# Kernel tuning notes

Measured on AMD Instinct MI355X. Metric: run time of the kernel, lower is better.

## Reference

```python
import jax, jax.numpy as jnp
import numpy as np

LOG_2PI = float(np.log(2.0 * np.pi))


def setup_inputs() -> dict:
    key = jax.random.key(0)
    k1, k2, k3 = jax.random.split(key, 3)
    N, M, D = 8192, 4096, 784
    samples = jax.random.normal(k1, (N, D), dtype=jnp.float32)
    x = jax.random.normal(k2, (M, D), dtype=jnp.float32)
    # per-feature std, kept away from zero for numerical sanity
    std = jax.random.uniform(k3, (D,), dtype=jnp.float32, minval=0.5, maxval=1.5)
    return {"samples": samples, "x": x, "std": std}


def reference(samples, x, std):
    # Diagonal-Gaussian mixture log-prob:
    #   logp[n, m] = sum_d [ -0.5*((s_nd - x_md)/std_d)^2 - 0.5*log(2*pi) - log(std_d) ]
    # computed via the ||u||^2 + ||v||^2 - 2 u.v identity on std-scaled vectors
    # (mathematically identical to the torch broadcast, without the (N,M,D) tensor).
    N, D = samples.shape
    M = x.shape[0]
    u = samples / std  # (N, D)
    v = x / std        # (M, D)
    sq_dist = (
        jnp.sum(u * u, axis=1)[:, None]
        + jnp.sum(v * v, axis=1)[None, :]
        - 2.0 * jnp.einsum("nd,md->nm", u, v)
    )  # (N, M)
    log_const = -0.5 * D * LOG_2PI - jnp.sum(jnp.log(std))
    log_prob = -0.5 * sq_dist + log_const  # (N, M)
    # logsumexp over mixture components, minus log(M)
    return jax.nn.logsumexp(log_prob, axis=1) - jnp.log(jnp.asarray(M, dtype=samples.dtype))
```

## Files before the change

kernel.cpp:

```cpp
#include <hip/hip_runtime.h>
#include <cstdint>
#include <cstddef>


#define N_ROWS 8192
#define M_ROWS 4096
#define D_DIM  784
#define KPB    896
#define LOG2PI 1.8378770664093453f
#define LOGM   8.317766166719343f

typedef unsigned char u8;
typedef __attribute__((ext_vector_type(8))) int   i32x8;
typedef __attribute__((ext_vector_type(4))) float f32x4;

__device__ __forceinline__ void gld16(const u8* g, u8* l) {
    __builtin_amdgcn_global_load_lds(
        (__attribute__((address_space(1))) void*)(void*)g,
        (__attribute__((address_space(3))) void*)l, 16, 0, 0);
}

__global__ __launch_bounds__(256) void k_prep(const float* __restrict__ samples,
                                              const float* __restrict__ x,
                                              const float* __restrict__ stdv,
                                              u8* __restrict__ dst,
                                              float* __restrict__ norm) {
    const int wid = threadIdx.x >> 6, lane = threadIdx.x & 63;
    const int row0 = blockIdx.x * 8 + wid * 2;

    float4 rstd[4];
#pragma unroll
    for (int i = 0; i < 4; ++i) {
        int c = lane + 64 * i;
        rstd[i] = make_float4(1.f, 1.f, 1.f, 1.f);
        if (c < 196) {
            float4 d = ((const float4*)stdv)[c];
            rstd[i] = make_float4(1.f / d.x, 1.f / d.y, 1.f / d.z, 1.f / d.w);
        }
    }

#pragma unroll
    for (int rr = 0; rr < 2; ++rr) {
        const int row = row0 + rr;
        const float* src = (row < N_ROWS) ? samples + (size_t)row * D_DIM
                                          : x + (size_t)(row - N_ROWS) * D_DIM;
        unsigned* drow = (unsigned*)(dst + (size_t)row * KPB);
        float sq = 0.f;
#pragma unroll
        for (int i = 0; i < 4; ++i) {
            const int c = lane + 64 * i;
            if (c < 224) {
                unsigned p = 0;
                if (c < 196) {
                    float4 s = ((const float4*)src)[c];
                    float ux = s.x * rstd[i].x, uy = s.y * rstd[i].y;
                    float uz = s.z * rstd[i].z, uw = s.w * rstd[i].w;
                    p = __builtin_amdgcn_cvt_pk_fp8_f32(ux, uy, 0, false);
                    p = __builtin_amdgcn_cvt_pk_fp8_f32(uz, uw, p, true);
                    float r0 = __builtin_amdgcn_cvt_f32_fp8(p, 0);
                    float r1 = __builtin_amdgcn_cvt_f32_fp8(p, 1);
                    float r2 = __builtin_amdgcn_cvt_f32_fp8(p, 2);
                    float r3 = __builtin_amdgcn_cvt_f32_fp8(p, 3);
                    sq += r0 * r0 + r1 * r1 + r2 * r2 + r3 * r3;
                }
                drow[c] = p;
            }
        }
        for (int m = 32; m; m >>= 1) sq += __shfl_xor(sq, m);
        if (lane == 0) norm[row] = sq;
    }
}

__global__ __launch_bounds__(256) void k_gemm(const u8* __restrict__ U,
                                              const u8* __restrict__ V,
                                              const float* __restrict__ vnorm,
                                              float* __restrict__ pmax,
                                              float* __restrict__ psum) {
    __shared__ __align__(16) char smem[65536];
    float2* part = (float2*)smem;

    const int tid = threadIdx.x;
    const int lane = tid & 63;
    const int wid = tid >> 6;
    const int waveRow = wid >> 1;
    const int waveCol = wid & 1;
    const int bCol = blockIdx.x;
    const int bRow = blockIdx.y;
    const int g = lane >> 4, rl = lane & 15;

    const int r16 = lane >> 2, sl = lane & 3;
    const int gc16 = sl ^ ((r16 >> 1) & 3);
    const u8* ga[4]; const u8* gb[4]; int loff[4];
#pragma unroll
    for (int t = 0; t < 4; ++t) {
        const int lin = wid * 4 + t, h = lin & 1, rg = lin >> 1;
        ga[t] = U + (size_t)(bRow * 128 + rg * 16 + r16) * KPB + h * 64 + gc16 * 16;
        gb[t] = V + (size_t)(bCol * 128 + rg * 16 + r16) * KPB + h * 64 + gc16 * 16;
        loff[t] = h * 8192 + rg * 1024;
    }

    const int key = (rl >> 1) & 3;
    const int hA = (g >> 1) * 8192;
    const int slotLo = (2 * (g & 1)) ^ key;
    const int aoff = hA + (waveRow * 64 + rl) * 64 + slotLo * 16;
    const int boff = 16384 + hA + (waveCol * 64 + rl) * 64 + slotLo * 16;

    f32x4 acc[4][4];
#pragma unroll
    for (int i = 0; i < 4; ++i)
#pragma unroll
        for (int j = 0; j < 4; ++j) acc[i][j] = (f32x4){0.f, 0.f, 0.f, 0.f};

#pragma unroll
    for (int t = 0; t < 4; ++t) gld16(ga[t], (u8*)(smem + loff[t]));
#pragma unroll
    for (int t = 0; t < 4; ++t) gld16(gb[t], (u8*)(smem + 16384 + loff[t]));

#pragma unroll
    for (int kt = 0; kt < 7; ++kt) {
        if (kt < 6) {
            char* nb = smem + ((kt + 1) & 1) * 32768;
            const int k1 = (kt + 1) * 128;
#pragma unroll
            for (int t = 0; t < 4; ++t) gld16(ga[t] + k1, (u8*)(nb + loff[t]));
#pragma unroll
            for (int t = 0; t < 4; ++t) gld16(gb[t] + k1, (u8*)(nb + 16384 + loff[t]));
            __builtin_amdgcn_s_waitcnt(0x0F78);
        } else {
            __builtin_amdgcn_s_waitcnt(0x0F70);
        }
        __builtin_amdgcn_s_barrier();

        const char* base = smem + (kt & 1) * 32768;
        i32x8 a[4], b[4];
#pragma unroll
        for (int i = 0; i < 4; ++i) {
            int4 L = *(const int4*)(base + (aoff + i * 1024));
            int4 H = *(const int4*)(base + ((aoff + i * 1024) ^ 16));
            a[i] = (i32x8){L.x, L.y, L.z, L.w, H.x, H.y, H.z, H.w};
        }
#pragma unroll
        for (int j = 0; j < 4; ++j) {
            int4 L = *(const int4*)(base + (boff + j * 1024));
            int4 H = *(const int4*)(base + ((boff + j * 1024) ^ 16));
            b[j] = (i32x8){L.x, L.y, L.z, L.w, H.x, H.y, H.z, H.w};
        }
#pragma unroll
        for (int i = 0; i < 4; ++i)
#pragma unroll
            for (int j = 0; j < 4; ++j)
                acc[i][j] = __builtin_amdgcn_mfma_scale_f32_16x16x128_f8f6f4(
                    a[i], b[j], acc[i][j], 0 , 0 ,
                    0, 127 , 0, 127 );

        __builtin_amdgcn_s_barrier();
    }
    __syncthreads();

    float vn[4];
#pragma unroll
    for (int j = 0; j < 4; ++j) vn[j] = vnorm[bCol * 128 + waveCol * 64 + j * 16 + rl];

    const int prow0 = waveRow * 64 + g * 4;
    const int pcol = waveCol * 16 + rl;
#pragma unroll
    for (int i = 0; i < 4; ++i) {
#pragma unroll
        for (int rg = 0; rg < 4; ++rg) {
            float w0 = acc[i][0][rg] - 0.5f * vn[0];
            float w1 = acc[i][1][rg] - 0.5f * vn[1];
            float w2 = acc[i][2][rg] - 0.5f * vn[2];
            float w3 = acc[i][3][rg] - 0.5f * vn[3];
            float m = fmaxf(fmaxf(w0, w1), fmaxf(w2, w3));
            float s = __expf(w0 - m) + __expf(w1 - m) + __expf(w2 - m) + __expf(w3 - m);
            part[(prow0 + i * 16 + rg) * 33 + pcol] = make_float2(m, s);
        }
    }
    __syncthreads();
    if (tid < 128) {
        const float2* p = part + tid * 33;
        float m = p[0].x;
#pragma unroll
        for (int c = 1; c < 32; ++c) m = fmaxf(m, p[c].x);
        float s = 0.f;
#pragma unroll
        for (int c = 0; c < 32; ++c) { float2 q = p[c]; s += q.y * __expf(q.x - m); }
        size_t grow = (size_t)(bRow * 128 + tid);
        pmax[grow * 32 + bCol] = m;
        psum[grow * 32 + bCol] = s;
    }
}

__global__ __launch_bounds__(256) void k_final(const float* __restrict__ pmax,
                                               const float* __restrict__ psum,
                                               const float* __restrict__ norm,
                                               const float* __restrict__ stdv,
                                               float* __restrict__ out) {
    __shared__ float wsum[4];
    const int t = threadIdx.x;
    float ls = 0.f;
    for (int d = t; d < D_DIM; d += 256) ls += logf(stdv[d]);
    for (int m = 32; m; m >>= 1) ls += __shfl_xor(ls, m);
    if ((t & 63) == 0) wsum[t >> 6] = ls;
    __syncthreads();
    const float logc = -0.5f * (float)D_DIM * LOG2PI - (wsum[0] + wsum[1] + wsum[2] + wsum[3]);

    const int n = blockIdx.x * 256 + t;
    const float* pm = pmax + (size_t)n * 32;
    const float* ps = psum + (size_t)n * 32;
    float gm = pm[0];
#pragma unroll
    for (int c = 1; c < 32; ++c) gm = fmaxf(gm, pm[c]);
    float S = 0.f;
#pragma unroll
    for (int c = 0; c < 32; ++c) S += ps[c] * __expf(pm[c] - gm);
    out[n] = gm + logf(S) - 0.5f * norm[n] + logc - LOGM;
}

extern "C" void kernel_launch(void* const* d_in, const int* in_sizes, int n_in,
                              void* d_out, int out_size, void* d_ws, size_t ws_size,
                              hipStream_t stream) {
    const float* samples = (const float*)d_in[0];
    const float* x       = (const float*)d_in[1];
    const float* stdv    = (const float*)d_in[2];
    float* out = (float*)d_out;

    char* ws = (char*)d_ws;
    u8*    U    = (u8*)ws;
    u8*    V    = (u8*)(ws + 7340032);
    float* norm = (float*)(ws + 11010048);
    float* pmax = (float*)(ws + 11059200);
    float* psum = (float*)(ws + 12107776);

    k_prep<<<(N_ROWS + M_ROWS) / 8, 256, 0, stream>>>(samples, x, stdv, U, norm);
    k_gemm<<<dim3(M_ROWS / 128, N_ROWS / 128), 256, 0, stream>>>(U, V, norm + N_ROWS, pmax, psum);
    k_final<<<N_ROWS / 256, 256, 0, stream>>>(pmax, psum, norm, stdv, out);
}
```

Before: 126.0 us.

## Enlarge GEMM tile to 256x256 with 8 waves and deeper LDS pipeline

The fp8 MFMA GEMM goes from 128x128 tiles with 4 waves to 256x256 tiles with 8 waves, each wave computing 128x64. LDS grows to 128KB, split into four 64-wide K half-buffers, and K-step loads are issued further ahead. The MFMA loop is split into phases with barriers and s_setprio. The larger tile halves global traffic per FLOP and the number of partial logsumexp columns, at the cost of heavy LDS use, likely one block per CU, and only 512 blocks.

```diff
diff --git a/kernel.cpp b/kernel.cpp
--- a/kernel.cpp
+++ b/kernel.cpp
@@ -71,100 +71,107 @@
     }
 }
 
-__global__ __launch_bounds__(256) void k_gemm(const u8* __restrict__ U,
-                                              const u8* __restrict__ V,
-                                              const float* __restrict__ vnorm,
-                                              float* __restrict__ pmax,
-                                              float* __restrict__ psum) {
-    __shared__ __align__(16) char smem[65536];
+__global__ __launch_bounds__(512, 2) void k_gemm(const u8* __restrict__ U,
+                                                 const u8* __restrict__ V,
+                                                 const float* __restrict__ vnorm,
+                                                 float* __restrict__ pmax,
+                                                 float* __restrict__ psum) {
+    __shared__ __align__(16) char smem[131072];
     float2* part = (float2*)smem;
 
     const int tid = threadIdx.x;
     const int lane = tid & 63;
     const int wid = tid >> 6;
-    const int waveRow = wid >> 1;
-    const int waveCol = wid & 1;
+    const int waveRow = wid >> 2;
+    const int waveCol = wid & 3;
     const int bCol = blockIdx.x;
     const int bRow = blockIdx.y;
     const int g = lane >> 4, rl = lane & 15;
 
     const int r16 = lane >> 2, sl = lane & 3;
     const int gc16 = sl ^ ((r16 >> 1) & 3);
-    const u8* ga[4]; const u8* gb[4]; int loff[4];
-#pragma unroll
-    for (int t = 0; t < 4; ++t) {
-        const int lin = wid * 4 + t, h = lin & 1, rg = lin >> 1;
-        ga[t] = U + (size_t)(bRow * 128 + rg * 16 + r16) * KPB + h * 64 + gc16 * 16;
-        gb[t] = V + (size_t)(bCol * 128 + rg * 16 + r16) * KPB + h * 64 + gc16 * 16;
-        loff[t] = h * 8192 + rg * 1024;
+    const u8* gA[2]; const u8* gB[2]; int lo[2];
+#pragma unroll
+    for (int q = 0; q < 2; ++q) {
+        const int rg = wid * 2 + q;
+        gA[q] = U + (size_t)(bRow * 256 + rg * 16 + r16) * KPB + gc16 * 16;
+        gB[q] = V + (size_t)(bCol * 256 + rg * 16 + r16) * KPB + gc16 * 16;
+        lo[q] = rg * 1024;
     }
 
     const int key = (rl >> 1) & 3;
-    const int hA = (g >> 1) * 8192;
     const int slotLo = (2 * (g & 1)) ^ key;
-    const int aoff = hA + (waveRow * 64 + rl) * 64 + slotLo * 16;
-    const int boff = 16384 + hA + (waveCol * 64 + rl) * 64 + slotLo * 16;
-
-    f32x4 acc[4][4];
-#pragma unroll
-    for (int i = 0; i < 4; ++i)
+    const int aoff = (g >> 1) * 32768 + (waveRow * 128 + rl) * 64 + slotLo * 16;
+    const int boff = (g >> 1) * 32768 + 16384 + (waveCol * 64 + rl) * 64 + slotLo * 16;
+
+    f32x4 acc[8][4];
+#pragma unroll
+    for (int i = 0; i < 8; ++i)
 #pragma unroll
         for (int j = 0; j < 4; ++j) acc[i][j] = (f32x4){0.f, 0.f, 0.f, 0.f};
 
-#pragma unroll
-    for (int t = 0; t < 4; ++t) gld16(ga[t], (u8*)(smem + loff[t]));
-#pragma unroll
-    for (int t = 0; t < 4; ++t) gld16(gb[t], (u8*)(smem + 16384 + loff[t]));
-
-#pragma unroll
-    for (int kt = 0; kt < 7; ++kt) {
-        if (kt < 6) {
-            char* nb = smem + ((kt + 1) & 1) * 32768;
-            const int k1 = (kt + 1) * 128;
-#pragma unroll
-            for (int t = 0; t < 4; ++t) gld16(ga[t] + k1, (u8*)(nb + loff[t]));
-#pragma unroll
-            for (int t = 0; t < 4; ++t) gld16(gb[t] + k1, (u8*)(nb + 16384 + loff[t]));
-            __builtin_amdgcn_s_waitcnt(0x0F78);
-        } else {
-            __builtin_amdgcn_s_waitcnt(0x0F70);
-        }
+#define ISSUE(u) { \
+    u8* lb = (u8*)smem + ((u) & 3) * 32768; \
+    const int ko = (u) * 64; \
+    gld16(gA[0] + ko, lb + lo[0]); \
+    gld16(gB[0] + ko, lb + 16384 + lo[0]); \
+    gld16(gA[1] + ko, lb + lo[1]); \
+    gld16(gB[1] + ko, lb + 16384 + lo[1]); }
+
+    ISSUE(0); ISSUE(1); ISSUE(2);
+
+#pragma unroll
+    for (int T = 0; T < 7; ++T) {
+        if (T < 6) ISSUE(2 * T + 3);
+        if (T < 6) __builtin_amdgcn_s_waitcnt(0x0F78);
+        else       __builtin_amdgcn_s_waitcnt(0x0F70);
         __builtin_amdgcn_s_barrier();
 
-        const char* base = smem + (kt & 1) * 32768;
-        i32x8 a[4], b[4];
-#pragma unroll
-        for (int i = 0; i < 4; ++i) {
-            int4 L = *(const int4*)(base + (aoff + i * 1024));
-            int4 H = *(const int4*)(base + ((aoff + i * 1024) ^ 16));
-            a[i] = (i32x8){L.x, L.y, L.z, L.w, H.x, H.y, H.z, H.w};
-        }
-#pragma unroll
-        for (int j = 0; j < 4; ++j) {
-            int4 L = *(const int4*)(base + (boff + j * 1024));
-            int4 H = *(const int4*)(base + ((boff + j * 1024) ^ 16));
-            b[j] = (i32x8){L.x, L.y, L.z, L.w, H.x, H.y, H.z, H.w};
-        }
-#pragma unroll
-        for (int i = 0; i < 4; ++i)
-#pragma unroll
-            for (int j = 0; j < 4; ++j)
-                acc[i][j] = __builtin_amdgcn_mfma_scale_f32_16x16x128_f8f6f4(
-                    a[i], b[j], acc[i][j], 0 , 0 ,
-                    0, 127 , 0, 127 );
-
-        __builtin_amdgcn_s_barrier();
-    }
+        const char* base = smem + (T & 1) * 65536;
+        i32x8 b[4], a[2];
+#pragma unroll
+        for (int ph = 0; ph < 4; ++ph) {
+            if (ph == 0) {
+#pragma unroll
+                for (int j = 0; j < 4; ++j) {
+                    int4 L = *(const int4*)(base + (boff + j * 1024));
+                    int4 H = *(const int4*)(base + ((boff + j * 1024) ^ 16));
+                    b[j] = (i32x8){L.x, L.y, L.z, L.w, H.x, H.y, H.z, H.w};
+                }
+            }
+#pragma unroll
+            for (int t = 0; t < 2; ++t) {
+                const int i = ph * 2 + t;
+                int4 L = *(const int4*)(base + (aoff + i * 1024));
+                int4 H = *(const int4*)(base + ((aoff + i * 1024) ^ 16));
+                a[t] = (i32x8){L.x, L.y, L.z, L.w, H.x, H.y, H.z, H.w};
+            }
+            __builtin_amdgcn_s_barrier();
+            __builtin_amdgcn_s_waitcnt(0xC07F);
+            __builtin_amdgcn_s_setprio(1);
+#pragma unroll
+            for (int t = 0; t < 2; ++t)
+#pragma unroll
+                for (int j = 0; j < 4; ++j)
+                    acc[ph * 2 + t][j] = __builtin_amdgcn_mfma_scale_f32_16x16x128_f8f6f4(
+                        a[t], b[j], acc[ph * 2 + t][j], 0 , 0 ,
+                        0, 127 , 0, 127 );
+            __builtin_amdgcn_s_setprio(0);
+            __builtin_amdgcn_s_barrier();
+        }
+        if (T < 5) ISSUE(2 * T + 4);
+    }
+#undef ISSUE
     __syncthreads();
 
     float vn[4];
 #pragma unroll
-    for (int j = 0; j < 4; ++j) vn[j] = vnorm[bCol * 128 + waveCol * 64 + j * 16 + rl];
-
-    const int prow0 = waveRow * 64 + g * 4;
-    const int pcol = waveCol * 16 + rl;
-#pragma unroll
-    for (int i = 0; i < 4; ++i) {
+    for (int j = 0; j < 4; ++j) vn[j] = vnorm[bCol * 256 + waveCol * 64 + j * 16 + rl];
+
+    const int prow0 = waveRow * 128 + g * 4;
+    const int pc = waveCol * 16 + rl;
+#pragma unroll
+    for (int i = 0; i < 8; ++i) {
 #pragma unroll
         for (int rg = 0; rg < 4; ++rg) {
             float w0 = acc[i][0][rg] - 0.5f * vn[0];
@@ -173,21 +180,22 @@
             float w3 = acc[i][3][rg] - 0.5f * vn[3];
             float m = fmaxf(fmaxf(w0, w1), fmaxf(w2, w3));
             float s = __expf(w0 - m) + __expf(w1 - m) + __expf(w2 - m) + __expf(w3 - m);
-            part[(prow0 + i * 16 + rg) * 33 + pcol] = make_float2(m, s);
+            part[(prow0 + i * 16 + rg) * 64 + pc] = make_float2(m, s);
         }
     }
     __syncthreads();
-    if (tid < 128) {
-        const float2* p = part + tid * 33;
-        float m = p[0].x;
-#pragma unroll
-        for (int c = 1; c < 32; ++c) m = fmaxf(m, p[c].x);
+    if (tid < 256) {
+        const float2* p = part + tid * 64;
+        const int rot = tid & 63;
+        float m = -3.4e38f;
+#pragma unroll 8
+        for (int q = 0; q < 64; ++q) m = fmaxf(m, p[(q + rot) & 63].x);
         float s = 0.f;
-#pragma unroll
-        for (int c = 0; c < 32; ++c) { float2 q = p[c]; s += q.y * __expf(q.x - m); }
-        size_t grow = (size_t)(bRow * 128 + tid);
-        pmax[grow * 32 + bCol] = m;
-        psum[grow * 32 + bCol] = s;
+#pragma unroll 8
+        for (int q = 0; q < 64; ++q) { float2 v = p[(q + rot) & 63]; s += v.y * __expf(v.x - m); }
+        size_t grow = (size_t)(bRow * 256 + tid);
+        pmax[grow * 16 + bCol] = m;
+        psum[grow * 16 + bCol] = s;
     }
 }
 
@@ -206,14 +214,14 @@
     const float logc = -0.5f * (float)D_DIM * LOG2PI - (wsum[0] + wsum[1] + wsum[2] + wsum[3]);
 
     const int n = blockIdx.x * 256 + t;
-    const float* pm = pmax + (size_t)n * 32;
-    const float* ps = psum + (size_t)n * 32;
+    const float* pm = pmax + (size_t)n * 16;
+    const float* ps = psum + (size_t)n * 16;
     float gm = pm[0];
 #pragma unroll
-    for (int c = 1; c < 32; ++c) gm = fmaxf(gm, pm[c]);
+    for (int c = 1; c < 16; ++c) gm = fmaxf(gm, pm[c]);
     float S = 0.f;
 #pragma unroll
-    for (int c = 0; c < 32; ++c) S += ps[c] * __expf(pm[c] - gm);
+    for (int c = 0; c < 16; ++c) S += ps[c] * __expf(pm[c] - gm);
     out[n] = gm + logf(S) - 0.5f * norm[n] + logc - LOGM;
 }
 
@@ -230,9 +238,9 @@
     u8*    V    = (u8*)(ws + 7340032);
     float* norm = (float*)(ws + 11010048);
     float* pmax = (float*)(ws + 11059200);
-    float* psum = (float*)(ws + 12107776);
+    float* psum = (float*)(ws + 11583488);
 
     k_prep<<<(N_ROWS + M_ROWS) / 8, 256, 0, stream>>>(samples, x, stdv, U, norm);
-    k_gemm<<<dim3(M_ROWS / 128, N_ROWS / 128), 256, 0, stream>>>(U, V, norm + N_ROWS, pmax, psum);
+    k_gemm<<<dim3(M_ROWS / 256, N_ROWS / 256), 512, 0, stream>>>(U, V, norm + N_ROWS, pmax, psum);
     k_final<<<N_ROWS / 256, 256, 0, stream>>>(pmax, psum, norm, stdv, out);
 }
```

New measurement: 139.2 us. 10.5% more time.
